# Kernel tuning notes

Hardware: AMD Instinct MI355X
Metric: run time of the kernel (lower is better)

The kernel has to match this reference:

```python
import jax, jax.numpy as jnp
import numpy as np

D_LATENTS = 256
B, N = 8, 4096
EPS = 1e-5  # BatchNorm eps (torch default)


def _w(k, shape):
    return jax.random.normal(k, shape, jnp.float32) * 0.05


def setup_inputs() -> dict:
    key = jax.random.key(0)
    ks = jax.random.split(key, 20)
    d4, d2, d = D_LATENTS // 4, D_LATENTS // 2, D_LATENTS
    def bn(k):
        k1, k2 = jax.random.split(k)
        g = 1.0 + 0.1 * jax.random.normal(k1, (0,), jnp.float32)  # placeholder
        return g
    inp = {
        "x": jax.random.normal(ks[0], (B, 3, N), jnp.float32),
        "conv1_w": _w(ks[1], (d4, 3)),
        "bn1_g": 1.0 + 0.1 * jax.random.normal(ks[2], (d4,), jnp.float32),
        "bn1_b": 0.1 * jax.random.normal(ks[3], (d4,), jnp.float32),
        "conv2_w": _w(ks[4], (d4, d4)),
        "bn2_g": 1.0 + 0.1 * jax.random.normal(ks[5], (d4,), jnp.float32),
        "bn2_b": 0.1 * jax.random.normal(ks[6], (d4,), jnp.float32),
        "le0_w1": _w(ks[7], (d2, d2)),
        "le0_g1": 1.0 + 0.1 * jax.random.normal(ks[8], (d2,), jnp.float32),
        "le0_b1": 0.1 * jax.random.normal(ks[9], (d2,), jnp.float32),
        "le0_w2": _w(ks[10], (d2, d2)),
        "le0_g2": 1.0 + 0.1 * jax.random.normal(ks[11], (d2,), jnp.float32),
        "le0_b2": 0.1 * jax.random.normal(ks[12], (d2,), jnp.float32),
        "le1_w1": _w(ks[13], (d, d)),
        "le1_g1": 1.0 + 0.1 * jax.random.normal(ks[14], (d,), jnp.float32),
        "le1_b1": 0.1 * jax.random.normal(ks[15], (d,), jnp.float32),
        "le1_w2": _w(ks[16], (d, d)),
        "le1_g2": 1.0 + 0.1 * jax.random.normal(ks[17], (d,), jnp.float32),
        "le1_b2": 0.1 * jax.random.normal(ks[18], (d,), jnp.float32),
    }
    return inp


def _bn_relu(y, g, b, axes, ch_axis):
    # BatchNorm (training-mode batch stats, biased var like torch) + ReLU
    m = jnp.mean(y, axes, keepdims=True)
    v = jnp.var(y, axes, keepdims=True)
    shp = [1] * y.ndim
    shp[ch_axis] = -1
    return jax.nn.relu((y - m) * jax.lax.rsqrt(v + EPS) * g.reshape(shp) + b.reshape(shp))


def _square_distance(src, dst):
    # src [B,S,3], dst [B,N,3] -> [B,S,N]
    return (jnp.sum(src * src, -1, keepdims=True)
            - 2.0 * jnp.einsum('bsc,bnc->bsn', src, dst)
            + jnp.sum(dst * dst, -1)[:, None, :])


def _fps(xyz, npoint):
    # farthest point sampling, deterministic start at index 0
    Bb, Nn, _ = xyz.shape
    def step(carry, _):
        dist_min, farthest = carry
        centroid = jnp.take_along_axis(xyz, farthest[:, None, None], axis=1)  # [B,1,3]
        d = jnp.sum((xyz - centroid) ** 2, -1)  # [B,N]
        dist_min = jnp.minimum(dist_min, d)
        nxt = jnp.argmax(dist_min, -1).astype(jnp.int32)
        return (dist_min, nxt), farthest
    init = (jnp.full((Bb, Nn), 1e10, xyz.dtype), jnp.zeros((Bb,), jnp.int32))
    _, idxs = jax.lax.scan(step, init, None, length=npoint)
    return jnp.transpose(idxs)  # [B, npoint]


def _sample_and_group(npoint, nsample, xyz, points):
    # PCT-style: FPS centers, kNN neighbors (radius unused), concat(rel, center)
    Bb = xyz.shape[0]
    fps_idx = _fps(xyz, npoint)                       # [B,S]
    bidx = jnp.arange(Bb)[:, None]
    new_xyz = xyz[bidx, fps_idx]                      # [B,S,3]
    new_pts = points[bidx, fps_idx]                   # [B,S,D]
    d2 = _square_distance(new_xyz, xyz)               # [B,S,N]
    _, knn_idx = jax.lax.top_k(-d2, nsample)          # [B,S,ns]
    grouped = points[jnp.arange(Bb)[:, None, None], knn_idx]  # [B,S,ns,D]
    center = new_pts[:, :, None, :]
    feat = jnp.concatenate([grouped - center,
                            jnp.broadcast_to(center, grouped.shape)], axis=-1)
    return new_xyz, feat  # [B,S,3], [B,S,ns,2D]


def _local_encoder(x4, w1, g1, b1, w2, g2, b2):
    # x4: [b,n,s,d] -> conv1x1/bn/relu x2 over channel dim, max over s -> [b,out,n]
    y = jnp.einsum('bnsd,od->bnos', x4, w1)
    y = _bn_relu(y, g1, b1, (0, 1, 3), 2)
    y = jnp.einsum('bnis,oi->bnos', y, w2)
    y = _bn_relu(y, g2, b2, (0, 1, 3), 2)
    y = jnp.max(y, axis=3)                # [b,n,out]
    return jnp.transpose(y, (0, 2, 1))    # [b,out,n]


def reference(x, conv1_w, bn1_g, bn1_b, conv2_w, bn2_g, bn2_b,
              le0_w1, le0_g1, le0_b1, le0_w2, le0_g2, le0_b2,
              le1_w1, le1_g1, le1_b1, le1_w2, le1_g2, le1_b2):
    xyz = jnp.transpose(x, (0, 2, 1))                 # [B,N,3]
    y = jnp.einsum('bcn,oc->bon', x, conv1_w)
    y = _bn_relu(y, bn1_g, bn1_b, (0, 2), 1)
    y = jnp.einsum('bcn,oc->bon', y, conv2_w)
    y = _bn_relu(y, bn2_g, bn2_b, (0, 2), 1)
    pts = jnp.transpose(y, (0, 2, 1))                 # [B,N,d4]
    new_xyz, feat = _sample_and_group(512, 32, xyz, pts)       # [B,512,32,d2]
    f0 = _local_encoder(feat, le0_w1, le0_g1, le0_b1, le0_w2, le0_g2, le0_b2)  # [B,d2,512]
    pts1 = jnp.transpose(f0, (0, 2, 1))
    _, feat2 = _sample_and_group(256, 32, new_xyz, pts1)       # [B,256,32,d]
    f1 = _local_encoder(feat2, le1_w1, le1_g1, le1_b1, le1_w2, le1_g2, le1_b2)  # [B,d,256]
    return f1
```

## Files before the change

kernel.cpp:

```cpp
#include <hip/hip_runtime.h>

constexpr int B_  = 8;
constexpr int N_  = 4096;
constexpr int NP1 = 512;
constexpr int NP2 = 256;
constexpr float EPS_ = 1e-5f;

typedef __attribute__((ext_vector_type(8))) short bhalf8;
typedef __attribute__((ext_vector_type(4))) float f32x4;

__device__ inline short f2bf(float f) {
  union { float fv; unsigned u; } v; v.fv = f;
  unsigned r = v.u + 0x7FFFu + ((v.u >> 16) & 1u);
  return (short)(r >> 16);
}

template<int CTRL>
__device__ inline void dpp_amax(unsigned &khi, unsigned &klo) {
  unsigned ohi = (unsigned)__builtin_amdgcn_mov_dpp((int)khi, CTRL, 0xF, 0xF, false);
  unsigned olo = (unsigned)__builtin_amdgcn_mov_dpp((int)klo, CTRL, 0xF, 0xF, false);
  if (ohi > khi || (ohi == khi && olo > klo)) { khi = ohi; klo = olo; }
}
__device__ inline void swz16_amax(unsigned &khi, unsigned &klo) {
  unsigned ohi = (unsigned)__builtin_amdgcn_ds_swizzle((int)khi, 0x401F);
  unsigned olo = (unsigned)__builtin_amdgcn_ds_swizzle((int)klo, 0x401F);
  if (ohi > khi || (ohi == khi && olo > klo)) { khi = ohi; klo = olo; }
}
__device__ inline void x32_amax(unsigned &khi, unsigned &klo) {
  unsigned ohi = (unsigned)__shfl_xor((int)khi, 32);
  unsigned olo = (unsigned)__shfl_xor((int)klo, 32);
  if (ohi > khi || (ohi == khi && olo > klo)) { khi = ohi; klo = olo; }
}
__device__ inline unsigned ford(float f) {
  unsigned u = __float_as_uint(f);
  return u ^ (((unsigned)((int)u >> 31)) | 0x80000000u);
}

constexpr int S_BN1 = 0;
constexpr int S_BN2 = 128;
constexpr int S_L0A = 256;
constexpr int S_L0B = 512;
constexpr int S_L1A = 768;
constexpr int S_L1B = 1280;
constexpr int S_TOTAL = 1792;

constexpr size_t OFF_T1   = 0;
constexpr size_t OFF_YBUF = OFF_T1   + 2097152;
constexpr size_t OFF_PTS1 = OFF_YBUF + 16777216;
constexpr size_t OFF_NXYZ = OFF_PTS1 + 524288;
constexpr size_t OFF_WT2C = OFF_NXYZ + 12288;
constexpr size_t OFF_BW0A = OFF_WT2C + 4096;
constexpr size_t OFF_BW0B = OFF_BW0A + 8192;
constexpr size_t OFF_BW1A = OFF_BW0B + 8192;
constexpr size_t OFF_BW1B = OFF_BW1A + 32768;
constexpr size_t OFF_STAT = OFF_BW1B + 32768;
constexpr size_t OFF_CNT  = OFF_STAT + S_TOTAL;
constexpr size_t OFF_INT  = OFF_CNT + 16;

__device__ inline void prep_elem(int idx, const float* __restrict__ conv2w,
                                 const float* __restrict__ w0a, const float* __restrict__ w0b,
                                 const float* __restrict__ w1a, const float* __restrict__ w1b,
                                 float* __restrict__ wt2c,
                                 short* __restrict__ b0a, short* __restrict__ b0b,
                                 short* __restrict__ b1a, short* __restrict__ b1b) {
  if (idx < 4096) { int d = idx >> 6, o = idx & 63; wt2c[idx] = conv2w[o*64 + d]; return; }
  idx -= 4096;
  const float* w; short* dst; int D;
  if      (idx <  2048) { w = w0a; dst = b0a; D = 128; }
  else if (idx <  4096) { w = w0b; dst = b0b; D = 128; idx -= 2048; }
  else if (idx < 12288) { w = w1a; dst = b1a; D = 256; idx -= 4096; }
  else                  { w = w1b; dst = b1b; D = 256; idx -= 12288; }
  int kblk = idx / D, o = idx % D;
  const float* src = w + (size_t)o*D + kblk*8;
  bhalf8 pk;
#pragma unroll
  for (int j = 0; j < 8; ++j) pk[j] = f2bf(src[j]);
  *(bhalf8*)&dst[(size_t)idx*8] = pk;
}

struct FpsSmem {
  float lx[4096], ly[4096], lz[4096];
  float sx[512], sy[512], sz[512];
  unsigned long long wk[2][8];
  int seli1[512];
  int seli2[256];
};
struct ConvSmem {
  float xs[3][64];
  float redS[4][64], redQ[4][64];
  float sc[64], sh[64];
  float at[64*68];
};

__global__ __launch_bounds__(256) void front_kernel(
    const float* __restrict__ x,
    const float* __restrict__ conv1w, const float* __restrict__ bn1g, const float* __restrict__ bn1b,
    const float* __restrict__ conv2w, const float* __restrict__ bn2g, const float* __restrict__ bn2b,
    const float* __restrict__ w0a, const float* __restrict__ w0b,
    const float* __restrict__ w1a, const float* __restrict__ w1b,
    float* __restrict__ wt2c,
    short* __restrict__ b0a, short* __restrict__ b0b,
    short* __restrict__ b1a, short* __restrict__ b1b,
    float* __restrict__ t1, float* __restrict__ t2,
    float* __restrict__ stats, int* __restrict__ cnt,
    int* __restrict__ sel1, float* __restrict__ nxyz, int* __restrict__ sel2) {
  __shared__ __align__(16) char smem_raw[sizeof(FpsSmem)];
  int t = threadIdx.x;
  if (blockIdx.x < 8) {
    constexpr int NPTS = 4096, NSEL1 = 512, NSEL2 = 256, NT = 256;
    constexpr int K = NPTS / NT, NS = NT / 32;
    FpsSmem& S = *reinterpret_cast<FpsSmem*>(smem_raw);
    int b = blockIdx.x;
    int lane = t & 63, wid = t >> 6;
    const float* cb = x + (size_t)b * 3 * NPTS;
    for (int i = t; i < NPTS; i += NT) {
      S.lx[i] = cb[i]; S.ly[i] = cb[NPTS + i]; S.lz[i] = cb[2*NPTS + i];
    }
    __syncthreads();
    float px[K], py[K], pz[K], dm[K];
#pragma unroll
    for (int k = 0; k < K; ++k) {
      int p = t + k*NT;
      px[k] = S.lx[p]; py[k] = S.ly[p]; pz[k] = S.lz[p];
      dm[k] = 1e10f;
    }
    float cx = S.lx[0], cy = S.ly[0], cz = S.lz[0];
    if (t == 0) { S.seli1[0] = 0; S.sx[0] = cx; S.sy[0] = cy; S.sz[0] = cz; }
    for (int it = 1; it < NSEL1; ++it) {
      float bv = -1.f; int bi = 0;
#pragma unroll
      for (int k = 0; k < K; ++k) {
        float dx = px[k]-cx, dy = py[k]-cy, dz = pz[k]-cz;
        float d = dx*dx + dy*dy + dz*dz;
        float nd = fminf(dm[k], d);
        dm[k] = nd;
        if (nd > bv) { bv = nd; bi = t + k*NT; }
      }
      unsigned khi = __float_as_uint(bv), klo = ~(unsigned)bi;
      dpp_amax<0xB1>(khi, klo);
      dpp_amax<0x4E>(khi, klo);
      dpp_amax<0x141>(khi, klo);
      dpp_amax<0x140>(khi, klo);
      swz16_amax(khi, klo);
      int p = it & 1;
      if ((lane & 31) == 0)
        S.wk[p][wid*2 + (lane >> 5)] = ((unsigned long long)khi << 32) | klo;
      __syncthreads();
      unsigned long long best = S.wk[p][0];
#pragma unroll
      for (int i2 = 1; i2 < NS; ++i2) { unsigned long long v2 = S.wk[p][i2]; if (v2 > best) best = v2; }
      int Bi = (int)(~(unsigned)best);
      cx = S.lx[Bi]; cy = S.ly[Bi]; cz = S.lz[Bi];
      if (t == 0) { S.seli1[it] = Bi; S.sx[it] = cx; S.sy[it] = cy; S.sz[it] = cz; }
    }
    __syncthreads();
    if (t < 64) {
      constexpr int K2 = NSEL1 / 64;
      float qx[K2], qy[K2], qz[K2], dm2[K2];
#pragma unroll
      for (int k = 0; k < K2; ++k) {
        int p = t + k*64;
        qx[k] = S.sx[p]; qy[k] = S.sy[p]; qz[k] = S.sz[p];
        dm2[k] = 1e10f;
      }
      cx = S.sx[0]; cy = S.sy[0]; cz = S.sz[0];
      if (t == 0) S.seli2[0] = 0;
      for (int it = 1; it < NSEL2; ++it) {
        float bv = -1.f; int bi = 0;
#pragma unroll
        for (int k = 0; k < K2; ++k) {
          float dx = qx[k]-cx, dy = qy[k]-cy, dz = qz[k]-cz;
          float d = dx*dx + dy*dy + dz*dz;
          float nd = fminf(dm2[k], d);
          dm2[k] = nd;
          if (nd > bv) { bv = nd; bi = t + k*64; }
        }
        unsigned khi = __float_as_uint(bv), klo = ~(unsigned)bi;
        dpp_amax<0xB1>(khi, klo);
        dpp_amax<0x4E>(khi, klo);
        dpp_amax<0x141>(khi, klo);
        dpp_amax<0x140>(khi, klo);
        swz16_amax(khi, klo);
        x32_amax(khi, klo);
        int Bi = (int)~klo;
        cx = S.sx[Bi]; cy = S.sy[Bi]; cz = S.sz[Bi];
        if (t == 0) S.seli2[it] = Bi;
      }
    } else {
      for (int i = t - 64; i < NSEL1; i += NT - 64) {
        sel1[(size_t)b*NSEL1 + i] = S.seli1[i];
        float* q = nxyz + ((size_t)b*NSEL1 + i)*3;
        q[0] = S.sx[i]; q[1] = S.sy[i]; q[2] = S.sz[i];
      }
    }
    __syncthreads();
    for (int i = t; i < NSEL2; i += NT) sel2[(size_t)b*NSEL2 + i] = S.seli2[i];
    return;
  }
  ConvSmem& C = *reinterpret_cast<ConvSmem*>(smem_raw);
  int cb = blockIdx.x - 8;
  { int idx = cb*256 + t;
    if (idx < 24576) prep_elem(idx, conv2w, w0a, w0b, w1a, w1b, wt2c, b0a, b0b, b1a, b1b); }
  for (int tile = cb; tile < 512; tile += 256) {
    int b = tile >> 6, n0 = (tile & 63) << 6;
    if (t < 192) { int c = t >> 6, nl = t & 63; C.xs[c][nl] = x[((size_t)b*3 + c)*N_ + n0 + nl]; }
    __syncthreads();
    int o = t & 63, ng = t >> 6;
    float w0 = conv1w[o*3+0], w1 = conv1w[o*3+1], w2 = conv1w[o*3+2];
    float ls = 0.f, lq = 0.f;
#pragma unroll
    for (int k = 0; k < 16; ++k) {
      int nl = ng*16 + k;
      float y = C.xs[0][nl]*w0 + C.xs[1][nl]*w1 + C.xs[2][nl]*w2;
      t1[((size_t)b*N_ + n0 + nl)*64 + o] = y;
      ls += y; lq += y*y;
    }
    C.redS[ng][o] = ls; C.redQ[ng][o] = lq;
    __syncthreads();
    if (t < 64) {
      float s = C.redS[0][t]+C.redS[1][t]+C.redS[2][t]+C.redS[3][t];
      float q = C.redQ[0][t]+C.redQ[1][t]+C.redQ[2][t]+C.redQ[3][t];
      atomicAdd(&stats[S_BN1 + t], s);
      atomicAdd(&stats[S_BN1 + 64 + t], q);
    }
    __syncthreads();
  }
  if (t == 0) {
    __threadfence();
    __hip_atomic_fetch_add(&cnt[0], 1, __ATOMIC_ACQ_REL, __HIP_MEMORY_SCOPE_AGENT);
    while (__hip_atomic_load(&cnt[0], __ATOMIC_ACQUIRE, __HIP_MEMORY_SCOPE_AGENT) < 256)
      __builtin_amdgcn_s_sleep(8);
    __threadfence();
  }
  __syncthreads();
  if (t < 64) {
    float m = stats[S_BN1 + t] * (1.f/32768.f);
    float v = stats[S_BN1 + 64 + t] * (1.f/32768.f) - m*m;
    float s = bn1g[t] * rsqrtf(v + EPS_);
    C.sc[t] = s; C.sh[t] = bn1b[t] - m*s;
  }
  __syncthreads();
  for (int tile = cb; tile < 512; tile += 256) {
    int b = tile >> 6, n0 = (tile & 63) << 6;
    constexpr int P = 68;
    for (int e = t; e < 4096; e += 256) {
      int nl = e >> 6, c = e & 63;
      float v = t1[((size_t)b*N_ + n0 + nl)*64 + c];
      C.at[c*P + nl] = fmaxf(v*C.sc[c] + C.sh[c], 0.f);
    }
    __syncthreads();
    int o = t & 63, ng = t >> 6;
    float acc[16];
#pragma unroll
    for (int k = 0; k < 16; ++k) acc[k] = 0.f;
    for (int i = 0; i < 64; ++i) {
      float wv = wt2c[i*64 + o];
      const float* ar = &C.at[i*P + ng*16];
#pragma unroll
      for (int k = 0; k < 16; k += 4) {
        float4 a4 = *(const float4*)(ar + k);
        acc[k+0] += a4.x*wv; acc[k+1] += a4.y*wv;
        acc[k+2] += a4.z*wv; acc[k+3] += a4.w*wv;
      }
    }
    float ls = 0.f, lq = 0.f;
#pragma unroll
    for (int k = 0; k < 16; ++k) {
      float y = acc[k];
      t2[((size_t)b*N_ + n0 + ng*16 + k)*64 + o] = y;
      ls += y; lq += y*y;
    }
    C.redS[ng][o] = ls; C.redQ[ng][o] = lq;
    __syncthreads();
    if (t < 64) {
      float s = C.redS[0][t]+C.redS[1][t]+C.redS[2][t]+C.redS[3][t];
      float q = C.redQ[0][t]+C.redQ[1][t]+C.redQ[2][t]+C.redQ[3][t];
      atomicAdd(&stats[S_BN2 + t], s);
      atomicAdd(&stats[S_BN2 + 64 + t], q);
    }
    __syncthreads();
  }
  if (t == 0) {
    __threadfence();
    __hip_atomic_fetch_add(&cnt[1], 1, __ATOMIC_ACQ_REL, __HIP_MEMORY_SCOPE_AGENT);
    while (__hip_atomic_load(&cnt[1], __ATOMIC_ACQUIRE, __HIP_MEMORY_SCOPE_AGENT) < 256)
      __builtin_amdgcn_s_sleep(8);
    __threadfence();
  }
  __syncthreads();
  {
    int o = t & 63;
    float m = stats[S_BN2 + o] * (1.f/32768.f);
    float v = stats[S_BN2 + 64 + o] * (1.f/32768.f) - m*m;
    float s = bn2g[o] * rsqrtf(v + EPS_);
    float sh = bn2b[o] - m*s;
    for (int tile = cb; tile < 512; tile += 256)
#pragma unroll
      for (int j = 0; j < 16; ++j) {
        size_t idx = (size_t)tile*4096 + j*256 + t;
        t1[idx] = fmaxf(t2[idx]*s + sh, 0.f);
      }
  }
}

template<int NDST, int NQ, int NT, bool XLAY>
__global__ __launch_bounds__(NT) void knn_kernel(
    const float* __restrict__ dst, const float* __restrict__ nxyz,
    const int* __restrict__ qmap, int* __restrict__ knn_out) {
  constexpr int K  = NDST / NT;
  constexpr int NS = NT / 32;
  __shared__ unsigned long long wk[2][NS];
  __shared__ int kos[32];
  int blk = blockIdx.x, t = threadIdx.x;
  int b = blk / NQ, q = blk % NQ;
  int qrow = b*NP1 + (qmap ? qmap[b*NQ + q] : q);
  float qx = nxyz[qrow*3+0], qy = nxyz[qrow*3+1], qz = nxyz[qrow*3+2];
  float q2 = (qx*qx + qy*qy) + qz*qz;
  const float* db = dst + (size_t)b * (XLAY ? 3*NDST : NDST*3);
  float d2r[K];
#pragma unroll
  for (int k = 0; k < K; ++k) {
    int j = t + k*NT;
    float xx, yy, zz;
    if (XLAY) { xx = db[j]; yy = db[NDST + j]; zz = db[2*NDST + j]; }
    else      { xx = db[j*3]; yy = db[j*3+1]; zz = db[j*3+2]; }
    float dot = (qx*xx + qy*yy) + qz*zz;
    float p2  = (xx*xx + yy*yy) + zz*zz;
    d2r[k] = (q2 - 2.f*dot) + p2;
  }
  for (int r = 0; r < 32; ++r) {
    float bv = 3e38f; int bi = t;
#pragma unroll
    for (int k = 0; k < K; ++k) {
      float v = d2r[k];
      if (v < bv) { bv = v; bi = t + k*NT; }
    }
    unsigned khi = ~ford(bv), klo = ~(unsigned)bi;
    dpp_amax<0xB1>(khi, klo);
    dpp_amax<0x4E>(khi, klo);
    dpp_amax<0x141>(khi, klo);
    dpp_amax<0x140>(khi, klo);
    swz16_amax(khi, klo);
    int p = r & 1;
    if ((t & 31) == 0)
      wk[p][t >> 5] = ((unsigned long long)khi << 32) | klo;
    __syncthreads();
    unsigned long long best = wk[p][0];
#pragma unroll
    for (int i2 = 1; i2 < NS; ++i2) { unsigned long long v2 = wk[p][i2]; if (v2 > best) best = v2; }
    int Bi = (int)(~(unsigned)best);
    if (t == 0) kos[r] = Bi;
#pragma unroll
    for (int k = 0; k < K; ++k)
      if (t + k*NT == Bi) d2r[k] = 3e38f;
  }
  __syncthreads();
  if (t < 32) knn_out[((size_t)b*NQ + q)*32 + t] = kos[t];
}

template<int D, int PW, int NP, int SRCN, int SOFF>
__global__ __launch_bounds__(256) void gemm1_kernel(
    const float* __restrict__ pts, const int* __restrict__ knn,
    const int* __restrict__ cent, const short* __restrict__ bw,
    float* __restrict__ ybuf, float* __restrict__ stats) {
  constexpr int KB = D/8;
  __shared__ __align__(16) short As[64*D];
  __shared__ float cen_s[2*PW];
  __shared__ int kid_s[64];
  __shared__ float sstat[2*D];
  int t = threadIdx.x, blk = blockIdx.x;
  int g0 = blk*2;
  if (t < 64) {
    int grp = t >> 5, s = t & 31;
    kid_s[t] = knn[((size_t)(g0+grp))*32 + s];
  }
  for (int i = t; i < 2*PW; i += 256) {
    int grp = i / PW, d = i % PW;
    int g = g0 + grp; int b = g / NP; int ci = cent[g];
    cen_s[i] = pts[((size_t)b*SRCN + ci)*PW + d];
  }
  for (int i = t; i < 2*D; i += 256) sstat[i] = 0.f;
  __syncthreads();
  for (int task = t; task < 64*KB; task += 256) {
    int row = task / KB, c = task % KB;
    int grp = row >> 5;
    int g = g0 + grp; int b = g / NP;
    int d = c*8;
    float v0,v1,v2,v3,v4,v5,v6,v7;
    if (d < PW) {
      const float* src = pts + ((size_t)b*SRCN + kid_s[row])*PW + d;
      float4 x0 = *(const float4*)src, x1 = *(const float4*)(src+4);
      const float* cc = &cen_s[grp*PW + d];
      v0=x0.x-cc[0]; v1=x0.y-cc[1]; v2=x0.z-cc[2]; v3=x0.w-cc[3];
      v4=x1.x-cc[4]; v5=x1.y-cc[5]; v6=x1.z-cc[6]; v7=x1.w-cc[7];
    } else {
      const float* cc = &cen_s[grp*PW + d - PW];
      v0=cc[0]; v1=cc[1]; v2=cc[2]; v3=cc[3]; v4=cc[4]; v5=cc[5]; v6=cc[6]; v7=cc[7];
    }
    bhalf8 pk;
    pk[0]=f2bf(v0); pk[1]=f2bf(v1); pk[2]=f2bf(v2); pk[3]=f2bf(v3);
    pk[4]=f2bf(v4); pk[5]=f2bf(v5); pk[6]=f2bf(v6); pk[7]=f2bf(v7);
    int a16 = row*KB + (c ^ (row & 7));
    *(bhalf8*)&As[a16*8] = pk;
  }
  __syncthreads();
  int w = t >> 6, l = t & 63, lr = l & 15, lg = l >> 4;
  f32x4 acc[D/16];
#pragma unroll
  for (int ct = 0; ct < D/16; ++ct) acc[ct] = (f32x4){0.f,0.f,0.f,0.f};
  int r = w*16 + lr;
#pragma unroll
  for (int kg = 0; kg < D/32; ++kg) {
    int c = (kg*4 + lg) ^ (r & 7);
    bhalf8 af = *(const bhalf8*)&As[(r*KB + c)*8];
#pragma unroll
    for (int ct = 0; ct < D/16; ++ct) {
      bhalf8 bf = *(const bhalf8*)&bw[((size_t)(kg*4 + lg)*D + ct*16 + lr)*8];
      acc[ct] = __builtin_amdgcn_mfma_f32_16x16x32_bf16(af, bf, acc[ct], 0, 0, 0);
    }
  }
  size_t rb = (size_t)blk*64 + w*16 + lg*4;
#pragma unroll
  for (int ct = 0; ct < D/16; ++ct) {
    int col = ct*16 + lr;
    f32x4 a = acc[ct];
    float* yp = ybuf + rb*D + col;
    yp[0] = a[0]; yp[(size_t)D] = a[1]; yp[(size_t)2*D] = a[2]; yp[(size_t)3*D] = a[3];
    float s = a[0]+a[1]+a[2]+a[3];
    float q = a[0]*a[0]+a[1]*a[1]+a[2]*a[2]+a[3]*a[3];
    s += __shfl_xor(s, 16); q += __shfl_xor(q, 16);
    s += __shfl_xor(s, 32); q += __shfl_xor(q, 32);
    if (lg == 0) { atomicAdd(&sstat[col], s); atomicAdd(&sstat[D+col], q); }
  }
  __syncthreads();
  for (int i = t; i < 2*D; i += 256) atomicAdd(&stats[SOFF+i], sstat[i]);
}

template<int D, int SIN, int SOUT, int CNT>
__global__ __launch_bounds__(256) void gemm2_kernel(
    const float* __restrict__ g1, const float* __restrict__ b1,
    const short* __restrict__ bw, const float* __restrict__ ybuf,
    float* __restrict__ mm, float* __restrict__ stats) {
  __shared__ __align__(16) float scsh[2*D];
  __shared__ float sstat[2*D];
  __shared__ float wmax[4][D], wmin[4][D];
  int t = threadIdx.x, blk = blockIdx.x;
  for (int i = t; i < D; i += 256) {
    float m = stats[SIN + i] * (1.f/(float)CNT);
    float v = stats[SIN + D + i] * (1.f/(float)CNT) - m*m;
    float s = g1[i] * rsqrtf(v + EPS_);
    scsh[i] = s; scsh[D+i] = b1[i] - m*s;
  }
  for (int i = t; i < 2*D; i += 256) sstat[i] = 0.f;
  __syncthreads();
  int w = t >> 6, l = t & 63, lr = l & 15, lg = l >> 4;
  size_t row = (size_t)blk*64 + w*16 + lr;
  const float* yrow = ybuf + row*D;
  f32x4 acc[D/16];
#pragma unroll
  for (int ct = 0; ct < D/16; ++ct) acc[ct] = (f32x4){0.f,0.f,0.f,0.f};
#pragma unroll
  for (int kg = 0; kg < D/32; ++kg) {
    int k = kg*32 + lg*8;
    float4 y0 = *(const float4*)(yrow + k);
    float4 y1 = *(const float4*)(yrow + k + 4);
    bhalf8 af;
    af[0] = f2bf(fmaxf(y0.x*scsh[k+0] + scsh[D+k+0], 0.f));
    af[1] = f2bf(fmaxf(y0.y*scsh[k+1] + scsh[D+k+1], 0.f));
    af[2] = f2bf(fmaxf(y0.z*scsh[k+2] + scsh[D+k+2], 0.f));
    af[3] = f2bf(fmaxf(y0.w*scsh[k+3] + scsh[D+k+3], 0.f));
    af[4] = f2bf(fmaxf(y1.x*scsh[k+4] + scsh[D+k+4], 0.f));
    af[5] = f2bf(fmaxf(y1.y*scsh[k+5] + scsh[D+k+5], 0.f));
    af[6] = f2bf(fmaxf(y1.z*scsh[k+6] + scsh[D+k+6], 0.f));
    af[7] = f2bf(fmaxf(y1.w*scsh[k+7] + scsh[D+k+7], 0.f));
#pragma unroll
    for (int ct = 0; ct < D/16; ++ct) {
      bhalf8 bf = *(const bhalf8*)&bw[((size_t)(kg*4 + lg)*D + ct*16 + lr)*8];
      acc[ct] = __builtin_amdgcn_mfma_f32_16x16x32_bf16(af, bf, acc[ct], 0, 0, 0);
    }
  }
#pragma unroll
  for (int ct = 0; ct < D/16; ++ct) {
    int col = ct*16 + lr;
    f32x4 a = acc[ct];
    float mx = fmaxf(fmaxf(a[0], a[1]), fmaxf(a[2], a[3]));
    float mn = fminf(fminf(a[0], a[1]), fminf(a[2], a[3]));
    mx = fmaxf(mx, __shfl_xor(mx, 16)); mn = fminf(mn, __shfl_xor(mn, 16));
    mx = fmaxf(mx, __shfl_xor(mx, 32)); mn = fminf(mn, __shfl_xor(mn, 32));
    if (lg == 0) { wmax[w][col] = mx; wmin[w][col] = mn; }
    float s = a[0]+a[1]+a[2]+a[3];
    float q = a[0]*a[0]+a[1]*a[1]+a[2]*a[2]+a[3]*a[3];
    s += __shfl_xor(s, 16); q += __shfl_xor(q, 16);
    s += __shfl_xor(s, 32); q += __shfl_xor(q, 32);
    if (lg == 0) { atomicAdd(&sstat[col], s); atomicAdd(&sstat[D+col], q); }
  }
  __syncthreads();
  for (int i = t; i < 2*D; i += 256) {
    int g = i / D, col = i - g*D;
    float mx = fmaxf(wmax[2*g][col], wmax[2*g+1][col]);
    float mn = fminf(wmin[2*g][col], wmin[2*g+1][col]);
    float* mp = mm + ((size_t)blk*2 + g)*2*D;
    mp[col] = mx; mp[D + col] = mn;
    atomicAdd(&stats[SOUT+i], sstat[i]);
  }
}

template<int D, int NP, int SOFF, int CNT, bool TR>
__global__ __launch_bounds__(256) void le3_kernel(
    const float* __restrict__ g2, const float* __restrict__ b2,
    const float* __restrict__ mm, const float* __restrict__ stats,
    float* __restrict__ out) {
  int idx = blockIdx.x*256 + threadIdx.x;
  int g = idx / D, o = idx - g*D;
  float m = stats[SOFF + o] * (1.f/(float)CNT);
  float v = stats[SOFF + D + o] * (1.f/(float)CNT) - m*m;
  float s = g2[o] * rsqrtf(v + EPS_);
  float sh = b2[o] - m*s;
  const float* mp = mm + (size_t)g*2*D;
  float pick = (s >= 0.f) ? mp[o] : mp[D + o];
  float r = fmaxf(pick*s + sh, 0.f);
  if (TR) { int b = g / NP, n = g - b*NP; out[((size_t)b*D + o)*NP + n] = r; }
  else    out[(size_t)g*D + o] = r;
}

extern "C" void kernel_launch(void* const* d_in, const int* in_sizes, int n_in,
                              void* d_out, int out_size, void* d_ws, size_t ws_size,
                              hipStream_t stream) {
  (void)in_sizes; (void)n_in; (void)out_size; (void)ws_size;
  const float* x       = (const float*)d_in[0];
  const float* conv1_w = (const float*)d_in[1];
  const float* bn1_g   = (const float*)d_in[2];
  const float* bn1_b   = (const float*)d_in[3];
  const float* conv2_w = (const float*)d_in[4];
  const float* bn2_g   = (const float*)d_in[5];
  const float* bn2_b   = (const float*)d_in[6];
  const float* le0_w1  = (const float*)d_in[7];
  const float* le0_g1  = (const float*)d_in[8];
  const float* le0_b1  = (const float*)d_in[9];
  const float* le0_w2  = (const float*)d_in[10];
  const float* le0_g2  = (const float*)d_in[11];
  const float* le0_b2  = (const float*)d_in[12];
  const float* le1_w1  = (const float*)d_in[13];
  const float* le1_g1  = (const float*)d_in[14];
  const float* le1_b1  = (const float*)d_in[15];
  const float* le1_w2  = (const float*)d_in[16];
  const float* le1_g2  = (const float*)d_in[17];
  const float* le1_b2  = (const float*)d_in[18];

  float* ws   = (float*)d_ws;
  float* t1   = ws + OFF_T1;
  float* ybuf = ws + OFF_YBUF;
  float* t2   = ybuf;
  float* mm   = t1;
  float* pts1 = ws + OFF_PTS1;
  float* nxyz = ws + OFF_NXYZ;
  float* wt2c = ws + OFF_WT2C;
  short* bw0a = (short*)(ws + OFF_BW0A);
  short* bw0b = (short*)(ws + OFF_BW0B);
  short* bw1a = (short*)(ws + OFF_BW1A);
  short* bw1b = (short*)(ws + OFF_BW1B);
  float* stats = ws + OFF_STAT;
  int*   cnt   = (int*)(ws + OFF_CNT);
  int* fps1 = (int*)(ws + OFF_INT);
  int* fps2 = fps1 + 4096;
  int* knn1 = fps2 + 2048;
  int* knn2 = knn1 + 131072;

  hipMemsetAsync(stats, 0, (S_TOTAL + 16)*sizeof(float), stream);
  front_kernel<<<264, 256, 0, stream>>>(x,
      conv1_w, bn1_g, bn1_b, conv2_w, bn2_g, bn2_b,
      le0_w1, le0_w2, le1_w1, le1_w2,
      wt2c, bw0a, bw0b, bw1a, bw1b,
      t1, t2, stats, cnt, fps1, nxyz, fps2);

  knn_kernel<4096, 512, 256, true ><<<4096, 256, 0, stream>>>(x, nxyz, nullptr, knn1);
  knn_kernel< 512, 256, 256, false><<<2048, 256, 0, stream>>>(nxyz, nxyz, fps2, knn2);

  gemm1_kernel<128,  64, 512, 4096, S_L0A><<<2048, 256, 0, stream>>>(t1, knn1, fps1, bw0a, ybuf, stats);
  gemm2_kernel<128, S_L0A, S_L0B, 131072><<<2048, 256, 0, stream>>>(le0_g1, le0_b1, bw0b, ybuf, mm, stats);
  le3_kernel<128, 512, S_L0B, 131072, false><<<2048, 256, 0, stream>>>(le0_g2, le0_b2, mm, stats, pts1);

  gemm1_kernel<256, 128, 256,  512, S_L1A><<<1024, 256, 0, stream>>>(pts1, knn2, fps2, bw1a, ybuf, stats);
  gemm2_kernel<256, S_L1A, S_L1B, 65536><<<1024, 256, 0, stream>>>(le1_g1, le1_b1, bw1b, ybuf, mm, stats);
  le3_kernel<256, 256, S_L1B, 65536, true><<<2048, 256, 0, stream>>>(le1_g2, le1_b2, mm, stats, (float*)d_out);
}
```

Baseline: 973.0 us.

## Fuse KNN into front kernel using per-batch FPS ready flags

After: 1.040 ms. +6.9%, slower.

```diff
diff --git a/kernel.cpp b/kernel.cpp
--- a/kernel.cpp
+++ b/kernel.cpp
@@ -34,6 +34,21 @@
 __device__ inline unsigned ford(float f) {
   unsigned u = __float_as_uint(f);
   return u ^ (((unsigned)((int)u >> 31)) | 0x80000000u);
+}
+
+__device__ inline void set_flag_after_sync(int* f) {
+  if (threadIdx.x == 0) {
+    __threadfence();
+    __hip_atomic_store(f, 1, __ATOMIC_RELEASE, __HIP_MEMORY_SCOPE_AGENT);
+  }
+}
+__device__ inline void wait_flag(int* f) {
+  if (threadIdx.x == 0) {
+    while (__hip_atomic_load(f, __ATOMIC_ACQUIRE, __HIP_MEMORY_SCOPE_AGENT) == 0)
+      __builtin_amdgcn_s_sleep(8);
+    __threadfence();
+  }
+  __syncthreads();
 }
 
 constexpr int S_BN1 = 0;
@@ -55,7 +70,7 @@
 constexpr size_t OFF_BW1B = OFF_BW1A + 32768;
 constexpr size_t OFF_STAT = OFF_BW1B + 32768;
 constexpr size_t OFF_CNT  = OFF_STAT + S_TOTAL;
-constexpr size_t OFF_INT  = OFF_CNT + 16;
+constexpr size_t OFF_INT  = OFF_CNT + 32;
 
 __device__ inline void prep_elem(int idx, const float* __restrict__ conv2w,
                                  const float* __restrict__ w0a, const float* __restrict__ w0b,
@@ -91,6 +106,61 @@
   float sc[64], sh[64];
   float at[64*68];
 };
+struct KnnSmem {
+  unsigned long long wk[2][8];
+  int kos[32];
+};
+
+template<int NDST, bool XLAY>
+__device__ inline void knn_query(const float* __restrict__ db,
+                                 float qx, float qy, float qz,
+                                 int* __restrict__ out32, KnnSmem& Kn) {
+  constexpr int NT = 256;
+  constexpr int K  = NDST / NT;
+  constexpr int NS = NT / 32;
+  int t = threadIdx.x;
+  float q2 = (qx*qx + qy*qy) + qz*qz;
+  float d2r[K];
+#pragma unroll
+  for (int k = 0; k < K; ++k) {
+    int j = t + k*NT;
+    float xx, yy, zz;
+    if (XLAY) { xx = db[j]; yy = db[NDST + j]; zz = db[2*NDST + j]; }
+    else      { xx = db[j*3]; yy = db[j*3+1]; zz = db[j*3+2]; }
+    float dot = (qx*xx + qy*yy) + qz*zz;
+    float p2  = (xx*xx + yy*yy) + zz*zz;
+    d2r[k] = (q2 - 2.f*dot) + p2;
+  }
+  for (int r = 0; r < 32; ++r) {
+    float bv = 3e38f; int bi = t;
+#pragma unroll
+    for (int k = 0; k < K; ++k) {
+      float v = d2r[k];
+      if (v < bv) { bv = v; bi = t + k*NT; }
+    }
+    unsigned khi = ~ford(bv), klo = ~(unsigned)bi;
+    dpp_amax<0xB1>(khi, klo);
+    dpp_amax<0x4E>(khi, klo);
+    dpp_amax<0x141>(khi, klo);
+    dpp_amax<0x140>(khi, klo);
+    swz16_amax(khi, klo);
+    int p = r & 1;
+    if ((t & 31) == 0)
+      Kn.wk[p][t >> 5] = ((unsigned long long)khi << 32) | klo;
+    __syncthreads();
+    unsigned long long best = Kn.wk[p][0];
+#pragma unroll
+    for (int i2 = 1; i2 < NS; ++i2) { unsigned long long v2 = Kn.wk[p][i2]; if (v2 > best) best = v2; }
+    int Bi = (int)(~(unsigned)best);
+    if (t == 0) Kn.kos[r] = Bi;
+#pragma unroll
+    for (int k = 0; k < K; ++k)
+      if (t + k*NT == Bi) d2r[k] = 3e38f;
+  }
+  __syncthreads();
+  if (t < 32) out32[t] = Kn.kos[t];
+  __syncthreads();
+}
 
 __global__ __launch_bounds__(256) void front_kernel(
     const float* __restrict__ x,
@@ -103,7 +173,8 @@
     short* __restrict__ b1a, short* __restrict__ b1b,
     float* __restrict__ t1, float* __restrict__ t2,
     float* __restrict__ stats, int* __restrict__ cnt,
-    int* __restrict__ sel1, float* __restrict__ nxyz, int* __restrict__ sel2) {
+    int* __restrict__ sel1, float* __restrict__ nxyz, int* __restrict__ sel2,
+    int* __restrict__ knn1, int* __restrict__ knn2) {
   __shared__ __align__(16) char smem_raw[sizeof(FpsSmem)];
   int t = threadIdx.x;
   if (blockIdx.x < 8) {
@@ -154,6 +225,13 @@
       if (t == 0) { S.seli1[it] = Bi; S.sx[it] = cx; S.sy[it] = cy; S.sz[it] = cz; }
     }
     __syncthreads();
+    for (int i = t; i < NSEL1; i += NT) {
+      sel1[(size_t)b*NSEL1 + i] = S.seli1[i];
+      float* q = nxyz + ((size_t)b*NSEL1 + i)*3;
+      q[0] = S.sx[i]; q[1] = S.sy[i]; q[2] = S.sz[i];
+    }
+    __syncthreads();
+    set_flag_after_sync(&cnt[2 + b]);
     if (t < 64) {
       constexpr int K2 = NSEL1 / 64;
       float qx[K2], qy[K2], qz[K2], dm2[K2];
@@ -186,176 +264,141 @@
         cx = S.sx[Bi]; cy = S.sy[Bi]; cz = S.sz[Bi];
         if (t == 0) S.seli2[it] = Bi;
       }
-    } else {
-      for (int i = t - 64; i < NSEL1; i += NT - 64) {
-        sel1[(size_t)b*NSEL1 + i] = S.seli1[i];
-        float* q = nxyz + ((size_t)b*NSEL1 + i)*3;
-        q[0] = S.sx[i]; q[1] = S.sy[i]; q[2] = S.sz[i];
-      }
     }
     __syncthreads();
     for (int i = t; i < NSEL2; i += NT) sel2[(size_t)b*NSEL2 + i] = S.seli2[i];
+    __syncthreads();
+    set_flag_after_sync(&cnt[10 + b]);
     return;
   }
-  ConvSmem& C = *reinterpret_cast<ConvSmem*>(smem_raw);
-  int cb = blockIdx.x - 8;
-  { int idx = cb*256 + t;
-    if (idx < 24576) prep_elem(idx, conv2w, w0a, w0b, w1a, w1b, wt2c, b0a, b0b, b1a, b1b); }
-  for (int tile = cb; tile < 512; tile += 256) {
-    int b = tile >> 6, n0 = (tile & 63) << 6;
-    if (t < 192) { int c = t >> 6, nl = t & 63; C.xs[c][nl] = x[((size_t)b*3 + c)*N_ + n0 + nl]; }
-    __syncthreads();
-    int o = t & 63, ng = t >> 6;
-    float w0 = conv1w[o*3+0], w1 = conv1w[o*3+1], w2 = conv1w[o*3+2];
-    float ls = 0.f, lq = 0.f;
-#pragma unroll
-    for (int k = 0; k < 16; ++k) {
-      int nl = ng*16 + k;
-      float y = C.xs[0][nl]*w0 + C.xs[1][nl]*w1 + C.xs[2][nl]*w2;
-      t1[((size_t)b*N_ + n0 + nl)*64 + o] = y;
-      ls += y; lq += y*y;
-    }
-    C.redS[ng][o] = ls; C.redQ[ng][o] = lq;
+  if (blockIdx.x < 264) {
+    ConvSmem& C = *reinterpret_cast<ConvSmem*>(smem_raw);
+    int cb = blockIdx.x - 8;
+    { int idx = cb*256 + t;
+      if (idx < 24576) prep_elem(idx, conv2w, w0a, w0b, w1a, w1b, wt2c, b0a, b0b, b1a, b1b); }
+    for (int tile = cb; tile < 512; tile += 256) {
+      int b = tile >> 6, n0 = (tile & 63) << 6;
+      if (t < 192) { int c = t >> 6, nl = t & 63; C.xs[c][nl] = x[((size_t)b*3 + c)*N_ + n0 + nl]; }
+      __syncthreads();
+      int o = t & 63, ng = t >> 6;
+      float w0 = conv1w[o*3+0], w1 = conv1w[o*3+1], w2 = conv1w[o*3+2];
+      float ls = 0.f, lq = 0.f;
+#pragma unroll
+      for (int k = 0; k < 16; ++k) {
+        int nl = ng*16 + k;
+        float y = C.xs[0][nl]*w0 + C.xs[1][nl]*w1 + C.xs[2][nl]*w2;
+        t1[((size_t)b*N_ + n0 + nl)*64 + o] = y;
+        ls += y; lq += y*y;
+      }
+      C.redS[ng][o] = ls; C.redQ[ng][o] = lq;
+      __syncthreads();
+      if (t < 64) {
+        float s = C.redS[0][t]+C.redS[1][t]+C.redS[2][t]+C.redS[3][t];
+        float q = C.redQ[0][t]+C.redQ[1][t]+C.redQ[2][t]+C.redQ[3][t];
+        atomicAdd(&stats[S_BN1 + t], s);
+        atomicAdd(&stats[S_BN1 + 64 + t], q);
+      }
+      __syncthreads();
+    }
+    if (t == 0) {
+      __threadfence();
+      __hip_atomic_fetch_add(&cnt[0], 1, __ATOMIC_ACQ_REL, __HIP_MEMORY_SCOPE_AGENT);
+      while (__hip_atomic_load(&cnt[0], __ATOMIC_ACQUIRE, __HIP_MEMORY_SCOPE_AGENT) < 256)
+        __builtin_amdgcn_s_sleep(8);
+      __threadfence();
+    }
     __syncthreads();
     if (t < 64) {
-      float s = C.redS[0][t]+C.redS[1][t]+C.redS[2][t]+C.redS[3][t];
-      float q = C.redQ[0][t]+C.redQ[1][t]+C.redQ[2][t]+C.redQ[3][t];
-      atomicAdd(&stats[S_BN1 + t], s);
-      atomicAdd(&stats[S_BN1 + 64 + t], q);
-    }
-    __syncthreads();
-  }
-  if (t == 0) {
-    __threadfence();
-    __hip_atomic_fetch_add(&cnt[0], 1, __ATOMIC_ACQ_REL, __HIP_MEMORY_SCOPE_AGENT);
-    while (__hip_atomic_load(&cnt[0], __ATOMIC_ACQUIRE, __HIP_MEMORY_SCOPE_AGENT) < 256)
-      __builtin_amdgcn_s_sleep(8);
-    __threadfence();
-  }
-  __syncthreads();
-  if (t < 64) {
-    float m = stats[S_BN1 + t] * (1.f/32768.f);
-    float v = stats[S_BN1 + 64 + t] * (1.f/32768.f) - m*m;
-    float s = bn1g[t] * rsqrtf(v + EPS_);
-    C.sc[t] = s; C.sh[t] = bn1b[t] - m*s;
-  }
-  __syncthreads();
-  for (int tile = cb; tile < 512; tile += 256) {
-    int b = tile >> 6, n0 = (tile & 63) << 6;
-    constexpr int P = 68;
-    for (int e = t; e < 4096; e += 256) {
-      int nl = e >> 6, c = e & 63;
-      float v = t1[((size_t)b*N_ + n0 + nl)*64 + c];
-      C.at[c*P + nl] = fmaxf(v*C.sc[c] + C.sh[c], 0.f);
-    }
-    __syncthreads();
-    int o = t & 63, ng = t >> 6;
-    float acc[16];
-#pragma unroll
-    for (int k = 0; k < 16; ++k) acc[k] = 0.f;
-    for (int i = 0; i < 64; ++i) {
-      float wv = wt2c[i*64 + o];
-      const float* ar = &C.at[i*P + ng*16];
-#pragma unroll
-      for (int k = 0; k < 16; k += 4) {
-        float4 a4 = *(const float4*)(ar + k);
-        acc[k+0] += a4.x*wv; acc[k+1] += a4.y*wv;
-        acc[k+2] += a4.z*wv; acc[k+3] += a4.w*wv;
-      }
-    }
-    float ls = 0.f, lq = 0.f;
-#pragma unroll
-    for (int k = 0; k < 16; ++k) {
-      float y = acc[k];
-      t2[((size_t)b*N_ + n0 + ng*16 + k)*64 + o] = y;
-      ls += y; lq += y*y;
-    }
-    C.redS[ng][o] = ls; C.redQ[ng][o] = lq;
-    __syncthreads();
-    if (t < 64) {
-      float s = C.redS[0][t]+C.redS[1][t]+C.redS[2][t]+C.redS[3][t];
-      float q = C.redQ[0][t]+C.redQ[1][t]+C.redQ[2][t]+C.redQ[3][t];
-      atomicAdd(&stats[S_BN2 + t], s);
-      atomicAdd(&stats[S_BN2 + 64 + t], q);
-    }
-    __syncthreads();
-  }
-  if (t == 0) {
-    __threadfence();
-    __hip_atomic_fetch_add(&cnt[1], 1, __ATOMIC_ACQ_REL, __HIP_MEMORY_SCOPE_AGENT);
-    while (__hip_atomic_load(&cnt[1], __ATOMIC_ACQUIRE, __HIP_MEMORY_SCOPE_AGENT) < 256)
-      __builtin_amdgcn_s_sleep(8);
-    __threadfence();
-  }
-  __syncthreads();
-  {
-    int o = t & 63;
-    float m = stats[S_BN2 + o] * (1.f/32768.f);
-    float v = stats[S_BN2 + 64 + o] * (1.f/32768.f) - m*m;
-    float s = bn2g[o] * rsqrtf(v + EPS_);
-    float sh = bn2b[o] - m*s;
-    for (int tile = cb; tile < 512; tile += 256)
-#pragma unroll
-      for (int j = 0; j < 16; ++j) {
-        size_t idx = (size_t)tile*4096 + j*256 + t;
-        t1[idx] = fmaxf(t2[idx]*s + sh, 0.f);
-      }
-  }
-}
-
-template<int NDST, int NQ, int NT, bool XLAY>
-__global__ __launch_bounds__(NT) void knn_kernel(
-    const float* __restrict__ dst, const float* __restrict__ nxyz,
-    const int* __restrict__ qmap, int* __restrict__ knn_out) {
-  constexpr int K  = NDST / NT;
-  constexpr int NS = NT / 32;
-  __shared__ unsigned long long wk[2][NS];
-  __shared__ int kos[32];
-  int blk = blockIdx.x, t = threadIdx.x;
-  int b = blk / NQ, q = blk % NQ;
-  int qrow = b*NP1 + (qmap ? qmap[b*NQ + q] : q);
-  float qx = nxyz[qrow*3+0], qy = nxyz[qrow*3+1], qz = nxyz[qrow*3+2];
-  float q2 = (qx*qx + qy*qy) + qz*qz;
-  const float* db = dst + (size_t)b * (XLAY ? 3*NDST : NDST*3);
-  float d2r[K];
-#pragma unroll
-  for (int k = 0; k < K; ++k) {
-    int j = t + k*NT;
-    float xx, yy, zz;
-    if (XLAY) { xx = db[j]; yy = db[NDST + j]; zz = db[2*NDST + j]; }
-    else      { xx = db[j*3]; yy = db[j*3+1]; zz = db[j*3+2]; }
-    float dot = (qx*xx + qy*yy) + qz*zz;
-    float p2  = (xx*xx + yy*yy) + zz*zz;
-    d2r[k] = (q2 - 2.f*dot) + p2;
-  }
-  for (int r = 0; r < 32; ++r) {
-    float bv = 3e38f; int bi = t;
-#pragma unroll
-    for (int k = 0; k < K; ++k) {
-      float v = d2r[k];
-      if (v < bv) { bv = v; bi = t + k*NT; }
-    }
-    unsigned khi = ~ford(bv), klo = ~(unsigned)bi;
-    dpp_amax<0xB1>(khi, klo);
-    dpp_amax<0x4E>(khi, klo);
-    dpp_amax<0x141>(khi, klo);
-    dpp_amax<0x140>(khi, klo);
-    swz16_amax(khi, klo);
-    int p = r & 1;
-    if ((t & 31) == 0)
-      wk[p][t >> 5] = ((unsigned long long)khi << 32) | klo;
-    __syncthreads();
-    unsigned long long best = wk[p][0];
-#pragma unroll
-    for (int i2 = 1; i2 < NS; ++i2) { unsigned long long v2 = wk[p][i2]; if (v2 > best) best = v2; }
-    int Bi = (int)(~(unsigned)best);
-    if (t == 0) kos[r] = Bi;
-#pragma unroll
-    for (int k = 0; k < K; ++k)
-      if (t + k*NT == Bi) d2r[k] = 3e38f;
-  }
-  __syncthreads();
-  if (t < 32) knn_out[((size_t)b*NQ + q)*32 + t] = kos[t];
+      float m = stats[S_BN1 + t] * (1.f/32768.f);
+      float v = stats[S_BN1 + 64 + t] * (1.f/32768.f) - m*m;
+      float s = bn1g[t] * rsqrtf(v + EPS_);
+      C.sc[t] = s; C.sh[t] = bn1b[t] - m*s;
+    }
+    __syncthreads();
+    for (int tile = cb; tile < 512; tile += 256) {
+      int b = tile >> 6, n0 = (tile & 63) << 6;
+      constexpr int P = 68;
+      for (int e = t; e < 4096; e += 256) {
+        int nl = e >> 6, c = e & 63;
+        float v = t1[((size_t)b*N_ + n0 + nl)*64 + c];
+        C.at[c*P + nl] = fmaxf(v*C.sc[c] + C.sh[c], 0.f);
+      }
+      __syncthreads();
+      int o = t & 63, ng = t >> 6;
+      float acc[16];
+#pragma unroll
+      for (int k = 0; k < 16; ++k) acc[k] = 0.f;
+      for (int i = 0; i < 64; ++i) {
+        float wv = wt2c[i*64 + o];
+        const float* ar = &C.at[i*P + ng*16];
+#pragma unroll
+        for (int k = 0; k < 16; k += 4) {
+          float4 a4 = *(const float4*)(ar + k);
+          acc[k+0] += a4.x*wv; acc[k+1] += a4.y*wv;
+          acc[k+2] += a4.z*wv; acc[k+3] += a4.w*wv;
+        }
+      }
+      float ls = 0.f, lq = 0.f;
+#pragma unroll
+      for (int k = 0; k < 16; ++k) {
+        float y = acc[k];
+        t2[((size_t)b*N_ + n0 + ng*16 + k)*64 + o] = y;
+        ls += y; lq += y*y;
+      }
+      C.redS[ng][o] = ls; C.redQ[ng][o] = lq;
+      __syncthreads();
+      if (t < 64) {
+        float s = C.redS[0][t]+C.redS[1][t]+C.redS[2][t]+C.redS[3][t];
+        float q = C.redQ[0][t]+C.redQ[1][t]+C.redQ[2][t]+C.redQ[3][t];
+        atomicAdd(&stats[S_BN2 + t], s);
+        atomicAdd(&stats[S_BN2 + 64 + t], q);
+      }
+      __syncthreads();
+    }
+    if (t == 0) {
+      __threadfence();
+      __hip_atomic_fetch_add(&cnt[1], 1, __ATOMIC_ACQ_REL, __HIP_MEMORY_SCOPE_AGENT);
+      while (__hip_atomic_load(&cnt[1], __ATOMIC_ACQUIRE, __HIP_MEMORY_SCOPE_AGENT) < 256)
+        __builtin_amdgcn_s_sleep(8);
+      __threadfence();
+    }
+    __syncthreads();
+    {
+      int o = t & 63;
+      float m = stats[S_BN2 + o] * (1.f/32768.f);
+      float v = stats[S_BN2 + 64 + o] * (1.f/32768.f) - m*m;
+      float s = bn2g[o] * rsqrtf(v + EPS_);
+      float sh = bn2b[o] - m*s;
+      for (int tile = cb; tile < 512; tile += 256)
+#pragma unroll
+        for (int j = 0; j < 16; ++j) {
+          size_t idx = (size_t)tile*4096 + j*256 + t;
+          t1[idx] = fmaxf(t2[idx]*s + sh, 0.f);
+        }
+    }
+    __syncthreads();
+  }
+  KnnSmem& Kn = *reinterpret_cast<KnnSmem*>(smem_raw);
+  int w = blockIdx.x - 8;
+  int lastb = -1;
+  for (int q = w; q < 4096; q += 504) {
+    int b = q >> 9, qi = q & 511;
+    if (b != lastb) { wait_flag(&cnt[2 + b]); lastb = b; }
+    const float* qp = nxyz + ((size_t)b*NP1 + qi)*3;
+    float qx = qp[0], qy = qp[1], qz = qp[2];
+    knn_query<4096, true>(x + (size_t)b*3*N_, qx, qy, qz,
+                          knn1 + (size_t)q*32, Kn);
+  }
+  lastb = -1;
+  for (int q = w; q < 2048; q += 504) {
+    int b = q >> 8, qi = q & 255;
+    if (b != lastb) { wait_flag(&cnt[10 + b]); lastb = b; }
+    int qrow = b*NP1 + sel2[b*NP2 + qi];
+    const float* qp = nxyz + (size_t)qrow*3;
+    float qx = qp[0], qy = qp[1], qz = qp[2];
+    knn_query<512, false>(nxyz + (size_t)b*NP1*3, qx, qy, qz,
+                          knn2 + (size_t)q*32, Kn);
+  }
 }
 
 template<int D, int PW, int NP, int SRCN, int SOFF>
@@ -566,15 +609,12 @@
   int* knn1 = fps2 + 2048;
   int* knn2 = knn1 + 131072;
 
-  hipMemsetAsync(stats, 0, (S_TOTAL + 16)*sizeof(float), stream);
-  front_kernel<<<264, 256, 0, stream>>>(x,
+  hipMemsetAsync(stats, 0, (S_TOTAL + 32)*sizeof(float), stream);
+  front_kernel<<<512, 256, 0, stream>>>(x,
       conv1_w, bn1_g, bn1_b, conv2_w, bn2_g, bn2_b,
       le0_w1, le0_w2, le1_w1, le1_w2,
       wt2c, bw0a, bw0b, bw1a, bw1b,
-      t1, t2, stats, cnt, fps1, nxyz, fps2);
-
-  knn_kernel<4096, 512, 256, true ><<<4096, 256, 0, stream>>>(x, nxyz, nullptr, knn1);
-  knn_kernel< 512, 256, 256, false><<<2048, 256, 0, stream>>>(nxyz, nxyz, fps2, knn2);
+      t1, t2, stats, cnt, fps1, nxyz, fps2, knn1, knn2);
 
   gemm1_kernel<128,  64, 512, 4096, S_L0A><<<2048, 256, 0, stream>>>(t1, knn1, fps1, bw0a, ybuf, stats);
   gemm2_kernel<128, S_L0A, S_L0B, 131072><<<2048, 256, 0, stream>>>(le0_g1, le0_b1, bw0b, ybuf, mm, stats);
```

## Compute each KNN query with one wavefront and fuse both KNN launches

Applied to the files above, without the earlier changes.

New measurement: 926.7 us. 1.05x faster.

```diff
diff --git a/kernel.cpp b/kernel.cpp
--- a/kernel.cpp
+++ b/kernel.cpp
@@ -55,7 +55,7 @@
 constexpr size_t OFF_BW1B = OFF_BW1A + 32768;
 constexpr size_t OFF_STAT = OFF_BW1B + 32768;
 constexpr size_t OFF_CNT  = OFF_STAT + S_TOTAL;
-constexpr size_t OFF_INT  = OFF_CNT + 16;
+constexpr size_t OFF_INT  = OFF_CNT + 32;
 
 __device__ inline void prep_elem(int idx, const float* __restrict__ conv2w,
                                  const float* __restrict__ w0a, const float* __restrict__ w0b,
@@ -303,24 +303,17 @@
   }
 }
 
-template<int NDST, int NQ, int NT, bool XLAY>
-__global__ __launch_bounds__(NT) void knn_kernel(
-    const float* __restrict__ dst, const float* __restrict__ nxyz,
-    const int* __restrict__ qmap, int* __restrict__ knn_out) {
-  constexpr int K  = NDST / NT;
-  constexpr int NS = NT / 32;
-  __shared__ unsigned long long wk[2][NS];
-  __shared__ int kos[32];
-  int blk = blockIdx.x, t = threadIdx.x;
-  int b = blk / NQ, q = blk % NQ;
-  int qrow = b*NP1 + (qmap ? qmap[b*NQ + q] : q);
-  float qx = nxyz[qrow*3+0], qy = nxyz[qrow*3+1], qz = nxyz[qrow*3+2];
+template<int NDST, bool XLAY>
+__device__ inline void wave_knn(const float* __restrict__ db,
+                                float qx, float qy, float qz,
+                                int* __restrict__ out32) {
+  constexpr int K = NDST / 64;
+  int lane = threadIdx.x & 63;
   float q2 = (qx*qx + qy*qy) + qz*qz;
-  const float* db = dst + (size_t)b * (XLAY ? 3*NDST : NDST*3);
   float d2r[K];
 #pragma unroll
   for (int k = 0; k < K; ++k) {
-    int j = t + k*NT;
+    int j = lane + k*64;
     float xx, yy, zz;
     if (XLAY) { xx = db[j]; yy = db[NDST + j]; zz = db[2*NDST + j]; }
     else      { xx = db[j*3]; yy = db[j*3+1]; zz = db[j*3+2]; }
@@ -328,12 +321,13 @@
     float p2  = (xx*xx + yy*yy) + zz*zz;
     d2r[k] = (q2 - 2.f*dot) + p2;
   }
+  int myout = 0;
   for (int r = 0; r < 32; ++r) {
-    float bv = 3e38f; int bi = t;
+    float bv = 3e38f; int bi = lane;
 #pragma unroll
     for (int k = 0; k < K; ++k) {
       float v = d2r[k];
-      if (v < bv) { bv = v; bi = t + k*NT; }
+      if (v < bv) { bv = v; bi = lane + k*64; }
     }
     unsigned khi = ~ford(bv), klo = ~(unsigned)bi;
     dpp_amax<0xB1>(khi, klo);
@@ -341,21 +335,33 @@
     dpp_amax<0x141>(khi, klo);
     dpp_amax<0x140>(khi, klo);
     swz16_amax(khi, klo);
-    int p = r & 1;
-    if ((t & 31) == 0)
-      wk[p][t >> 5] = ((unsigned long long)khi << 32) | klo;
-    __syncthreads();
-    unsigned long long best = wk[p][0];
-#pragma unroll
-    for (int i2 = 1; i2 < NS; ++i2) { unsigned long long v2 = wk[p][i2]; if (v2 > best) best = v2; }
-    int Bi = (int)(~(unsigned)best);
-    if (t == 0) kos[r] = Bi;
+    x32_amax(khi, klo);
+    int Bi = (int)~klo;
+    if (lane == r) myout = Bi;
 #pragma unroll
     for (int k = 0; k < K; ++k)
-      if (t + k*NT == Bi) d2r[k] = 3e38f;
-  }
-  __syncthreads();
-  if (t < 32) knn_out[((size_t)b*NQ + q)*32 + t] = kos[t];
+      if (lane + k*64 == Bi) d2r[k] = 3e38f;
+  }
+  if (lane < 32) out32[lane] = myout;
+}
+
+__global__ __launch_bounds__(256) void knn_fused_kernel(
+    const float* __restrict__ x, const float* __restrict__ nxyz,
+    const int* __restrict__ sel2, int* __restrict__ knn1, int* __restrict__ knn2) {
+  int wid = threadIdx.x >> 6;
+  int blk = blockIdx.x;
+  if (blk < 1024) {
+    int q = blk*4 + wid;
+    int b = q >> 9, qi = q & 511;
+    const float* qp = nxyz + ((size_t)b*NP1 + qi)*3;
+    wave_knn<4096, true>(x + (size_t)b*3*N_, qp[0], qp[1], qp[2], knn1 + (size_t)q*32);
+  } else {
+    int q = (blk - 1024)*4 + wid;
+    int b = q >> 8, qi = q & 255;
+    int qrow = b*NP1 + sel2[b*NP2 + qi];
+    const float* qp = nxyz + (size_t)qrow*3;
+    wave_knn<512, false>(nxyz + (size_t)b*NP1*3, qp[0], qp[1], qp[2], knn2 + (size_t)q*32);
+  }
 }
 
 template<int D, int PW, int NP, int SRCN, int SOFF>
@@ -566,15 +572,14 @@
   int* knn1 = fps2 + 2048;
   int* knn2 = knn1 + 131072;
 
-  hipMemsetAsync(stats, 0, (S_TOTAL + 16)*sizeof(float), stream);
+  hipMemsetAsync(stats, 0, (S_TOTAL + 32)*sizeof(float), stream);
   front_kernel<<<264, 256, 0, stream>>>(x,
       conv1_w, bn1_g, bn1_b, conv2_w, bn2_g, bn2_b,
       le0_w1, le0_w2, le1_w1, le1_w2,
       wt2c, bw0a, bw0b, bw1a, bw1b,
       t1, t2, stats, cnt, fps1, nxyz, fps2);
 
-  knn_kernel<4096, 512, 256, true ><<<4096, 256, 0, stream>>>(x, nxyz, nullptr, knn1);
-  knn_kernel< 512, 256, 256, false><<<2048, 256, 0, stream>>>(nxyz, nxyz, fps2, knn2);
+  knn_fused_kernel<<<1536, 256, 0, stream>>>(x, nxyz, fps2, knn1, knn2);
 
   gemm1_kernel<128,  64, 512, 4096, S_L0A><<<2048, 256, 0, stream>>>(t1, knn1, fps1, bw0a, ybuf, stats);
   gemm2_kernel<128, S_L0A, S_L0B, 131072><<<2048, 256, 0, stream>>>(le0_g1, le0_b1, bw0b, ybuf, mm, stats);
```
